# Performance work log

Measured on AMD Instinct MI355X. Metric: run time of the kernel, lower is better.

Reference implementation:

```python
import jax, jax.numpy as jnp
import numpy as np

G, K1, K2, N, NP, EPS = 16, 128, 32, 128, 512, 1e-5

def _bn(x, axes):
    m = jnp.mean(x, axes, keepdims=True)
    v = jnp.var(x, axes, keepdims=True)  # biased, as torch BN training mode
    return (x - m) * jax.lax.rsqrt(v + EPS)

def _fps(xyz, npoint):
    # farthest point sampling, deterministic start at index 0; xyz (B,P,3)
    B, P, _ = xyz.shape
    def step(carry, _):
        dists, far = carry
        c = jnp.take_along_axis(xyz, far[:, None, None], axis=1)   # (B,1,3)
        d = jnp.sum((xyz - c) ** 2, -1)                            # (B,P)
        dists = jnp.minimum(dists, d)
        return (dists, jnp.argmax(dists, -1)), far
    init = (jnp.full((B, P), 1e10, xyz.dtype), jnp.zeros((B,), jnp.int32))
    _, idx = jax.lax.scan(step, init, None, length=npoint)         # (npoint,B)
    return jnp.take_along_axis(xyz, idx.T[:, :, None], axis=1)     # (B,npoint,3)

def _pointnet(x, w1, b1, w2, b2, w3, b3):
    h = jax.nn.relu(_bn(x @ w1 + b1, (0, 1)))
    h = jax.nn.relu(_bn(h @ w2 + b2, (0, 1)))
    h = _bn(h @ w3 + b3, (0, 1))
    return jnp.max(h, axis=1)                                      # (B,1024)

def _mapping(feat, w1, b1, w2, b2, w3, b3, w4, b4):
    # all 16 branches stacked on leading axis g
    h = jax.nn.relu(_bn(jnp.einsum('bk,gkj->gbj', feat, w1) + b1[:, None, :], (1,)))
    h = jax.nn.relu(_bn(jnp.einsum('gbj,gjk->gbk', h, w2) + b2[:, None, :], (1,)))
    h = jax.nn.relu(_bn(jnp.einsum('gbj,gjk->gbk', h, w3) + b3[:, None, :], (1,)))
    return jax.nn.relu(_bn(jnp.einsum('gbj,gjk->gbk', h, w4) + b4[:, None, :], (1,)))

def _axform(feat, fw, fb, c1w, c1b, c2w, c2b, c3w, c3b, c4w, c4b):
    # feat (G,B,K1); 1x1 convs expressed as einsums in channels-last layout
    xb = (jnp.einsum('gbk,gkm->gbm', feat, fw) + fb[:, None, :]).reshape(G, -1, N, K2)
    h = jax.nn.relu(_bn(jnp.einsum('gbnk,gkc->gbnc', xb, c1w) + c1b[:, None, None, :], (1, 2)))
    h = jax.nn.relu(_bn(jnp.einsum('gbnc,gcd->gbnd', h, c2w) + c2b[:, None, None, :], (1, 2)))
    h = jnp.einsum('gbnd,gde->gbne', h, c3w) + c3b[:, None, None, :]  # (G,B,N,1024)
    w = jax.nn.softmax(h, axis=2)                                     # softmax over N
    y = jnp.einsum('gbne,gbnk->gbek', w, xb)                          # (G,B,1024,K2)
    return jnp.einsum('gbek,gkc->gbec', y, c4w) + c4b[:, None, None, :]  # (G,B,1024,3)

def _forward(x, pn, mp, gen, ref):
    x_partial = _fps(x, NP)                                           # (B,512,3)
    feat = _pointnet(x, *pn)                                          # (B,1024)
    mfeat = _mapping(feat, *mp)                                       # (G,B,K1)
    x1g = _axform(mfeat, *gen)                                        # (G,B,1024,3)
    B = x.shape[0]
    x_1 = jnp.transpose(x1g, (1, 0, 2, 3)).reshape(B, -1, 3)          # (B,16384,3)
    fps1 = jax.vmap(lambda p: _fps(p, NP))(x1g)                       # (G,B,512,3)
    x_base = jnp.concatenate([fps1, jnp.broadcast_to(x_partial, (G,) + x_partial.shape)], axis=2)
    x2g = x_base + _axform(mfeat, *ref)                               # (G,B,1024,3)
    x_2 = jnp.transpose(x2g, (1, 0, 2, 3)).reshape(B, -1, 3)
    return x_1, x_2

def setup_inputs() -> dict:
    keys = iter(jax.random.split(jax.random.key(0), 40))
    def rn(shape, s=0.02):
        return (s * jax.random.normal(next(keys), shape)).astype(jnp.float32)
    inp = {}
    inp['x'] = jax.random.normal(next(keys), (16, 2048, 3), jnp.float32)
    inp['pn_w1'] = rn((3, 64));      inp['pn_b1'] = rn((64,))
    inp['pn_w2'] = rn((64, 128));    inp['pn_b2'] = rn((128,))
    inp['pn_w3'] = rn((128, 1024));  inp['pn_b3'] = rn((1024,))
    inp['mp_w1'] = rn((G, 1024, 1024)); inp['mp_b1'] = rn((G, 1024))
    inp['mp_w2'] = rn((G, 1024, 1024)); inp['mp_b2'] = rn((G, 1024))
    inp['mp_w3'] = rn((G, 1024, 1024)); inp['mp_b3'] = rn((G, 1024))
    inp['mp_w4'] = rn((G, 1024, K1));   inp['mp_b4'] = rn((G, K1))
    for p in ('g', 'r'):
        inp[p + '_fw'] = rn((G, K1, N * K2)); inp[p + '_fb'] = rn((G, N * K2))
        inp[p + '_c1w'] = rn((G, K2, 64));    inp[p + '_c1b'] = rn((G, 64))
        inp[p + '_c2w'] = rn((G, 64, 128));   inp[p + '_c2b'] = rn((G, 128))
        inp[p + '_c3w'] = rn((G, 128, 1024)); inp[p + '_c3b'] = rn((G, 1024))
        inp[p + '_c4w'] = rn((G, K2, 3));     inp[p + '_c4b'] = rn((G, 3))
    return inp

def reference(x, pn_w1, pn_b1, pn_w2, pn_b2, pn_w3, pn_b3,
              mp_w1, mp_b1, mp_w2, mp_b2, mp_w3, mp_b3, mp_w4, mp_b4,
              g_fw, g_fb, g_c1w, g_c1b, g_c2w, g_c2b, g_c3w, g_c3b, g_c4w, g_c4b,
              r_fw, r_fb, r_c1w, r_c1b, r_c2w, r_c2b, r_c3w, r_c3b, r_c4w, r_c4b):
    pn = (pn_w1, pn_b1, pn_w2, pn_b2, pn_w3, pn_b3)
    mp = (mp_w1, mp_b1, mp_w2, mp_b2, mp_w3, mp_b3, mp_w4, mp_b4)
    gen = (g_fw, g_fb, g_c1w, g_c1b, g_c2w, g_c2b, g_c3w, g_c3b, g_c4w, g_c4b)
    ref = (r_fw, r_fb, r_c1w, r_c1b, r_c2w, r_c2b, r_c3w, r_c3b, r_c4w, r_c4b)
    return _forward(x, pn, mp, gen, ref)
```

## Files before the change

kernel.cpp:

```cpp
#include <hip/hip_runtime.h>
#include <math.h>

#define TID ((int)threadIdx.x)

namespace {
constexpr float EPSf = 1e-5f;

struct FpsArgs {
  const float* pts; float* out; float* dmin; int* far;
  int it0, it1, nc;
};

__device__ __forceinline__ unsigned fenc(float f){
  unsigned u = __float_as_uint(f);
  return (u & 0x80000000u) ? ~u : (u | 0x80000000u);
}
__device__ __forceinline__ float fdec(unsigned e){
  unsigned u = (e & 0x80000000u) ? (e & 0x7fffffffu) : ~e;
  return __uint_as_float(u);
}

template<int CTRL>
__device__ __forceinline__ void dpp_comb(float& bm, int& bp){
  int om_i = __builtin_amdgcn_update_dpp(__float_as_int(bm), __float_as_int(bm), CTRL, 0xf, 0xf, false);
  int op   = __builtin_amdgcn_update_dpp(bp, bp, CTRL, 0xf, 0xf, false);
  float om = __int_as_float(om_i);
  if (om > bm || (om == bm && op < bp)){ bm = om; bp = op; }
}

template<int LP>
__device__ void fps_body(const FpsArgs& a, int ci){
  const int NPTS = 256*LP;
  const float* pts = a.pts + (size_t)ci * NPTS * 3;
  float* out = a.out + (size_t)ci * 512 * 3;
  float* dst = a.dmin + (size_t)ci * NPTS;
  float px[LP], py[LP], pz[LP], dmin[LP];
#pragma unroll
  for (int j = 0; j < LP; j++){
    int p = TID + 256*j;
    px[j] = pts[p*3+0]; py[j] = pts[p*3+1]; pz[j] = pts[p*3+2];
  }
  int far;
  if (a.it0 == 0){
#pragma unroll
    for (int j = 0; j < LP; j++) dmin[j] = 1e10f;
    far = 0;
  } else {
#pragma unroll
    for (int j = 0; j < LP; j++) dmin[j] = dst[TID + 256*j];
    far = a.far[ci];
  }
  __shared__ unsigned long long red2[2][4];
  for (int i = a.it0; i < a.it1; i++){
    float cx = pts[far*3+0], cy = pts[far*3+1], cz = pts[far*3+2];
    if (TID == 0){ out[i*3+0]=cx; out[i*3+1]=cy; out[i*3+2]=cz; }
    float bm = -1.f; int bp = 0;
#pragma unroll
    for (int j = 0; j < LP; j++){
      float dx = __fsub_rn(px[j], cx);
      float dy = __fsub_rn(py[j], cy);
      float dz = __fsub_rn(pz[j], cz);
      float d  = __fadd_rn(__fadd_rn(__fmul_rn(dx,dx), __fmul_rn(dy,dy)), __fmul_rn(dz,dz));
      float dm = fminf(dmin[j], d);
      dmin[j] = dm;
      if (dm > bm){ bm = dm; bp = TID + 256*j; }
    }
    dpp_comb<0x111>(bm,bp); dpp_comb<0x112>(bm,bp); dpp_comb<0x114>(bm,bp);
    dpp_comb<0x118>(bm,bp); dpp_comb<0x142>(bm,bp); dpp_comb<0x143>(bm,bp);
    unsigned long long key =
      ((unsigned long long)(unsigned)__builtin_amdgcn_readlane(__float_as_int(bm), 63) << 32)
      | (unsigned)~(unsigned)__builtin_amdgcn_readlane(bp, 63);
    if ((TID & 63) == 63) red2[i&1][TID>>6] = key;
    __syncthreads();
    unsigned long long k0=red2[i&1][0], k1=red2[i&1][1], k2=red2[i&1][2], k3=red2[i&1][3];
    k0 = k0>k1?k0:k1; k2 = k2>k3?k2:k3; k0 = k0>k2?k0:k2;
    far = (int)~(unsigned)k0;
  }
  if (a.it1 < 512){
#pragma unroll
    for (int j = 0; j < LP; j++) dst[TID + 256*j] = dmin[j];
    if (TID == 0) a.far[ci] = far;
  }
}

__device__ __forceinline__ int aswz64(int n, int k){
  return (n << 6) + ((((k >> 2) ^ ((n >> 3) & 3)) << 2) | (k & 3));
}
__device__ __forceinline__ int pswz(int n, int e){
  return (n << 6) + (e ^ (((n >> 3) & 3) << 3));
}

template<int C, int K, int FLP>
__global__ void __launch_bounds__(256) rowgemm_kernel(const float* __restrict__ in,
    const float* __restrict__ w, const float* __restrict__ bias, const float2* __restrict__ st2,
    float* __restrict__ out, int rows_per_g, FpsArgs fa)
{
  int bid = blockIdx.x;
  if constexpr (FLP > 0){
    if (bid < fa.nc){ fps_body<FLP>(fa, bid); return; }
    bid -= fa.nc;
  }
  constexpr int RPB = 256 / C;
  __shared__ float lin[RPB * K];
  size_t row0 = (size_t)bid * RPB;
  int g = (int)(row0 / rows_per_g);
  for (int i = TID; i < RPB*K; i += 256){
    float v = in[row0*(size_t)K + i];
    if (st2){ float2 s = st2[(size_t)g*K + (i % K)]; v = fmaxf((v - s.x)*s.y, 0.f); }
    lin[i] = v;
  }
  __syncthreads();
  int r = TID / C, c = TID % C;
  float acc = bias[(size_t)g*C + c];
  const float* wg = w + (size_t)g*K*C + c;
#pragma unroll
  for (int k = 0; k < K; k++) acc = fmaf(lin[r*K + k], wg[(size_t)k*C], acc);
  out[(row0 + r)*C + c] = acc;
}

template<int FLP>
__global__ void __launch_bounds__(256) big1024_kernel(const float* __restrict__ in,
    const float* __restrict__ w, const float* __restrict__ bias, const float2* __restrict__ st2,
    float* __restrict__ ps, float* __restrict__ pq,
    unsigned* __restrict__ maxenc, int rows_per_g, FpsArgs fa)
{
  int bid = blockIdx.x;
  if constexpr (FLP > 0){
    if (bid < fa.nc){ fps_body<FLP>(fa, bid); return; }
    bid -= fa.nc;
  }
  int rb = bid >> 1, ch = bid & 1;
  __shared__ float lin[32 * 128];
  size_t row0 = (size_t)rb * 32;
  int g = (int)(row0 / rows_per_g);
  for (int i = TID; i < 32*128; i += 256){
    float v = in[row0*128 + i];
    if (st2){ float2 s = st2[(size_t)g*128 + (i & 127)]; v = fmaxf((v - s.x)*s.y, 0.f); }
    lin[i] = v;
  }
  __syncthreads();
  int c0 = ch*512 + TID, c1 = c0 + 256;
  float a0[32], a1[32];
  float b0 = bias[(size_t)g*1024 + c0], b1 = bias[(size_t)g*1024 + c1];
#pragma unroll
  for (int r = 0; r < 32; r++){ a0[r] = b0; a1[r] = b1; }
  const float* wg = w + (size_t)g*128*1024;
  for (int k = 0; k < 128; k++){
    float w0 = wg[(size_t)k*1024 + c0];
    float w1 = wg[(size_t)k*1024 + c1];
#pragma unroll
    for (int r = 0; r < 32; r++){
      float lv = lin[r*128 + k];
      a0[r] = fmaf(lv, w0, a0[r]);
      a1[r] = fmaf(lv, w1, a1[r]);
    }
  }
  int b = (int)(row0 / 2048);
  float s0=0.f,q0=0.f,m0=-1e38f,s1=0.f,q1=0.f,m1=-1e38f;
#pragma unroll
  for (int r = 0; r < 32; r++){
    s0 += a0[r]; q0 = fmaf(a0[r],a0[r],q0); m0 = fmaxf(m0, a0[r]);
    s1 += a1[r]; q1 = fmaf(a1[r],a1[r],q1); m1 = fmaxf(m1, a1[r]);
  }
  ps[(size_t)rb*1024 + c0] = s0; pq[(size_t)rb*1024 + c0] = q0;
  ps[(size_t)rb*1024 + c1] = s1; pq[(size_t)rb*1024 + c1] = q1;
  atomicMax(&maxenc[(size_t)b*1024 + c0], fenc(m0));
  atomicMax(&maxenc[(size_t)b*1024 + c1], fenc(m1));
}

template<int FLP>
__global__ void __launch_bounds__(256) mapgemm_kernel(const float* __restrict__ in, int in_gstride,
    const float* __restrict__ w, const float* __restrict__ bias, const float2* __restrict__ st2,
    float* __restrict__ out, int K, int J, int JB, int NS, FpsArgs fa)
{
  int bid = blockIdx.x;
  if constexpr (FLP > 0){
    if (bid < fa.nc){ fps_body<FLP>(fa, bid); return; }
    bid -= fa.nc;
  }
  int kc = bid / (JB*16);
  int g  = (bid / JB) % 16;
  int jb = bid % JB;
  int j  = jb*256 + TID;
  bool jv = j < J;
  int jc = jv ? j : 0;
  int kchunk = K / NS;
  int k0 = kc * kchunk;
  __shared__ float lin[16 * 128];
  const float* ing = in + (size_t)g * in_gstride;
  float acc[16];
  float bv = (NS == 1 && jv) ? bias[(size_t)g*J + jc] : 0.f;
#pragma unroll
  for (int b = 0; b < 16; b++) acc[b] = bv;
  for (int kt = k0; kt < k0 + kchunk; kt += 128){
    __syncthreads();
    for (int i = TID; i < 2048; i += 256){
      int b = i >> 7, k = i & 127;
      float v = ing[(size_t)b*K + kt + k];
      if (st2){ float2 s = st2[(size_t)g*K + kt + k]; v = fmaxf((v - s.x)*s.y, 0.f); }
      lin[i] = v;
    }
    __syncthreads();
    const float* wg = w + ((size_t)g*K + kt)*J + jc;
    for (int k = 0; k < 128; k++){
      float wv = wg[(size_t)k*J];
#pragma unroll
      for (int b = 0; b < 16; b++) acc[b] = fmaf(lin[b*128 + k], wv, acc[b]);
    }
  }
  if (jv){
    if (NS == 1){
      for (int b = 0; b < 16; b++) out[((size_t)g*16 + b)*J + j] = acc[b];
    } else {
      for (int b = 0; b < 16; b++) out[(((size_t)kc*16 + g)*16 + b)*J + j] = acc[b];
    }
  }
}

__global__ void __launch_bounds__(256) redstats_kernel(const float* __restrict__ part,
    const float* __restrict__ bias, float* __restrict__ out, float2* __restrict__ st2,
    int J, int NS)
{
  int t = blockIdx.x*256 + TID;
  int g = t / J, j = t % J;
  float bv = bias[t];
  float s = 0.f, q = 0.f;
  for (int b = 0; b < 16; b++){
    float v = bv;
    for (int c = 0; c < NS; c++) v += part[(((size_t)c*16 + g)*16 + b)*J + j];
    out[((size_t)g*16 + b)*J + j] = v;
    s += v; q = fmaf(v, v, q);
  }
  float mean = s * (1.f/16.f);
  float var  = q * (1.f/16.f) - mean*mean;
  st2[t] = make_float2(mean, rsqrtf(fmaxf(var, 0.f) + EPSf));
}

__global__ void __launch_bounds__(256) statsacc_kernel(const float* __restrict__ in,
    float* __restrict__ part, int C, size_t chunk)
{
  size_t base = (size_t)blockIdx.x * chunk;
  int c = TID % C;
  float s = 0.f, q = 0.f;
  for (size_t idx = base + TID; idx < base + chunk; idx += 256){
    float v = in[idx]; s += v; q = fmaf(v, v, q);
  }
  __shared__ float ls[256], lq[256];
  ls[TID] = s; lq[TID] = q; __syncthreads();
  if (TID < C){
    for (int t = TID + C; t < 256; t += C){ s += ls[t]; q += lq[t]; }
    part[((size_t)blockIdx.x*C + c)*2]   = s;
    part[((size_t)blockIdx.x*C + c)*2+1] = q;
  }
}

__global__ void statsfin_kernel(const float* __restrict__ part, float2* __restrict__ st2,
    int C, int G, float invR)
{
  int slot = blockIdx.x*256 + TID;
  if (slot >= G*C) return;
  int g = slot / C, c = slot % C;
  int bpg = 256 / G;
  float s = 0.f, q = 0.f;
  for (int b = 0; b < bpg; b++){
    size_t p = ((size_t)(g*bpg + b)*C + c)*2;
    s += part[p]; q += part[p+1];
  }
  float mean = s*invR;
  float var  = q*invR - mean*mean;
  st2[slot] = make_float2(mean, rsqrtf(fmaxf(var, 0.f) + EPSf));
}

__global__ void pnfin_kernel(const float* __restrict__ ps, const float* __restrict__ pq,
                             float2* __restrict__ st)
{
  int c = blockIdx.x*256 + TID;
  float s = 0.f, q = 0.f;
  for (int rb = 0; rb < 1024; rb++){ s += ps[rb*1024 + c]; q += pq[rb*1024 + c]; }
  float mean = s * (1.f/32768.f);
  float var  = q * (1.f/32768.f) - mean*mean;
  st[c] = make_float2(mean, rsqrtf(fmaxf(var, 0.f) + EPSf));
}

__global__ void feat_kernel(const unsigned* __restrict__ me, const float2* __restrict__ st,
                            float* __restrict__ feat)
{
  int t = blockIdx.x*256 + TID;
  int c = t & 1023;
  float2 s = st[c];
  feat[t] = (fdec(me[t]) - s.x) * s.y;
}

template<int FLP>
__global__ void __launch_bounds__(256, 4) fused_kernel(const float* __restrict__ c2o,
    const float2* __restrict__ st2, const float* __restrict__ c3w,
    const float* __restrict__ xb, const float* __restrict__ c4w, const float* __restrict__ c4b,
    float* __restrict__ out_pts, float* __restrict__ out_x1, FpsArgs fa)
{
  int bid = blockIdx.x;
  if constexpr (FLP > 0){
    if (bid < fa.nc){ fps_body<FLP>(fa, bid); return; }
    bid -= fa.nc;
  }
  int gb = bid >> 3, eb = bid & 7;
  int g = gb >> 4, b = gb & 15;
  __shared__ float As[8192];
  __shared__ float xbl[4096];
  for (int i = TID; i < 4096; i += 256) xbl[i] = xb[(size_t)gb*4096 + i];

  int tn = TID >> 4, te = TID & 15;
  int n0 = tn*8, e0 = te*8;
  const float* wgp = c3w + ((size_t)g << 17) + eb*128 + e0;
  const float* src = c2o + (size_t)gb*16384;
  float h[8][8];
#pragma unroll
  for (int i = 0; i < 8; i++)
#pragma unroll
    for (int j = 0; j < 8; j++) h[i][j] = 0.f;

  for (int kh = 0; kh < 2; kh++){
    __syncthreads();
    for (int i = TID; i < 8192; i += 256){
      int n = i >> 6, k = i & 63;
      int kg = kh*64 + k;
      float2 s = st2[(size_t)g*128 + kg];
      As[aswz64(n,k)] = fmaxf((src[n*128 + kg] - s.x)*s.y, 0.f);
    }
    __syncthreads();
    for (int k4 = 0; k4 < 64; k4 += 4){
      float4 a[8];
#pragma unroll
      for (int i = 0; i < 8; i++) a[i] = *(const float4*)&As[aswz64(n0+i, k4)];
#pragma unroll
      for (int kk = 0; kk < 4; kk++){
        float4 wa = *(const float4*)(wgp + (size_t)(kh*64 + k4 + kk)*1024);
        float4 wb = *(const float4*)(wgp + (size_t)(kh*64 + k4 + kk)*1024 + 4);
#pragma unroll
        for (int i = 0; i < 8; i++){
          float av = (&a[i].x)[kk];
          h[i][0] = fmaf(av, wa.x, h[i][0]);
          h[i][1] = fmaf(av, wa.y, h[i][1]);
          h[i][2] = fmaf(av, wa.z, h[i][2]);
          h[i][3] = fmaf(av, wa.w, h[i][3]);
          h[i][4] = fmaf(av, wb.x, h[i][4]);
          h[i][5] = fmaf(av, wb.y, h[i][5]);
          h[i][6] = fmaf(av, wb.z, h[i][6]);
          h[i][7] = fmaf(av, wb.w, h[i][7]);
        }
      }
    }
  }

  for (int p = 0; p < 2; p++){
    __syncthreads();
    if ((te >> 3) == p){
      int el0 = (te & 7) * 8;
#pragma unroll
      for (int i = 0; i < 8; i++){
#pragma unroll
        for (int j4 = 0; j4 < 8; j4 += 4)
          *(float4*)&As[pswz(n0+i, el0+j4)] =
            make_float4(h[i][j4], h[i][j4+1], h[i][j4+2], h[i][j4+3]);
      }
    }
    __syncthreads();
    if (TID < 128){
      int el = TID >> 1, hh = TID & 1;
      float m = -1e38f;
      for (int jj = 0; jj < 64; jj++){
        int n = hh*64 + jj;
        m = fmaxf(m, As[pswz(n, el)]);
      }
      m = fmaxf(m, __shfl_xor(m, 1));
      float s = 0.f;
      float4 y[8];
#pragma unroll
      for (int q = 0; q < 8; q++) y[q] = make_float4(0.f,0.f,0.f,0.f);
      for (int jj = 0; jj < 64; jj++){
        int n = hh*64 + jj;
        float wv = __expf(As[pswz(n, el)] - m);
        s += wv;
        const float4* xr = (const float4*)&xbl[n*32];
#pragma unroll
        for (int q = 0; q < 8; q++){
          float4 xv = xr[q];
          y[q].x = fmaf(wv, xv.x, y[q].x);
          y[q].y = fmaf(wv, xv.y, y[q].y);
          y[q].z = fmaf(wv, xv.z, y[q].z);
          y[q].w = fmaf(wv, xv.w, y[q].w);
        }
      }
      s += __shfl_xor(s, 1);
#pragma unroll
      for (int q = 0; q < 8; q++){
        y[q].x += __shfl_xor(y[q].x, 1);
        y[q].y += __shfl_xor(y[q].y, 1);
        y[q].z += __shfl_xor(y[q].z, 1);
        y[q].w += __shfl_xor(y[q].w, 1);
      }
      if (hh == 0){
        const float* cw = c4w + g*96;
        float o0 = 0.f, o1 = 0.f, o2 = 0.f;
#pragma unroll
        for (int q = 0; q < 8; q++){
#pragma unroll
          for (int c2 = 0; c2 < 4; c2++){
            float yv = (&y[q].x)[c2];
            int k = q*4 + c2;
            o0 = fmaf(yv, cw[k*3+0], o0);
            o1 = fmaf(yv, cw[k*3+1], o1);
            o2 = fmaf(yv, cw[k*3+2], o2);
          }
        }
        float rs = 1.f / s;
        o0 = fmaf(rs, o0, c4b[g*3+0]);
        o1 = fmaf(rs, o1, c4b[g*3+1]);
        o2 = fmaf(rs, o2, c4b[g*3+2]);
        int eg = eb*128 + p*64 + el;
        size_t po = ((size_t)gb*1024 + eg)*3;
        out_pts[po+0] = o0; out_pts[po+1] = o1; out_pts[po+2] = o2;
        if (out_x1){
          size_t xo = (((size_t)b*16 + g)*1024 + eg)*3;
          out_x1[xo+0] = o0; out_x1[xo+1] = o1; out_x1[xo+2] = o2;
        }
      }
    }
  }
}

__global__ void combine_kernel(const float* __restrict__ fps1, const float* __restrict__ xpart,
                               const float* __restrict__ d2, float* __restrict__ x2)
{
  size_t i = (size_t)blockIdx.x*256 + TID;
  if (i >= (size_t)16*16*1024*3) return;
  int c = (int)(i % 3);
  size_t t = i / 3;
  int e = (int)(t % 1024);
  size_t gb = t / 1024;
  int g = (int)(gb >> 4), b = (int)(gb & 15);
  float base;
  if (e < 512) base = fps1[(gb*512 + e)*3 + c];
  else         base = xpart[((size_t)b*512 + (e - 512))*3 + c];
  x2[(((size_t)b*16384) + (size_t)g*1024 + e)*3 + c] = base + d2[i];
}

}

extern "C" void kernel_launch(void* const* d_in, const int* in_sizes, int n_in,
                              void* d_out, int out_size, void* d_ws, size_t ws_size,
                              hipStream_t stream)
{
  (void)in_sizes; (void)n_in; (void)out_size; (void)ws_size;
  const float* x    = (const float*)d_in[0];
  const float* pnw1 = (const float*)d_in[1];
  const float* pnb1 = (const float*)d_in[2];
  const float* pnw2 = (const float*)d_in[3];
  const float* pnb2 = (const float*)d_in[4];
  const float* pnw3 = (const float*)d_in[5];
  const float* pnb3 = (const float*)d_in[6];
  const float* mpw[4] = {(const float*)d_in[7],(const float*)d_in[9],(const float*)d_in[11],(const float*)d_in[13]};
  const float* mpb[4] = {(const float*)d_in[8],(const float*)d_in[10],(const float*)d_in[12],(const float*)d_in[14]};

  float* ws = (float*)d_ws;
  size_t o = 0;
  auto alloc = [&](size_t n){ float* p = ws + o; o += n; return p; };
  float* x_partial = alloc(24576);
  float* feat      = alloc(16384);
  float* mfeat     = alloc(32768);
  float2* st_pn1   = (float2*)alloc(128);
  float2* st_pn2   = (float2*)alloc(256);
  float2* st_pn3   = (float2*)alloc(2048);
  float2* st_c1    = (float2*)alloc(2048);
  float2* st_c2    = (float2*)alloc(4096);
  float2* st_map0  = (float2*)alloc(32768);
  float2* st_map1  = (float2*)alloc(32768);
  float2* st_map2  = (float2*)alloc(32768);
  float2* st_map3  = (float2*)alloc(4096);
  float* sa_part   = alloc(65536);
  float* pn_ps     = alloc(1048576);
  float* pn_pq     = alloc(1048576);
  unsigned* maxenc = (unsigned*)alloc(16384);
  float* mapA      = alloc(262144);
  float* mapB      = alloc(262144);
  float* mpart     = alloc(1048576);
  float* xb        = alloc(1048576);
  float* c1o       = alloc(2097152);
  float* c2o       = alloc(4194304);
  float* x1g       = alloc(786432);
  float* d2buf     = alloc(786432);
  float* fps1b     = alloc(393216);
  float* fpsA_dmin = alloc(32768);
  int*   fpsA_far  = (int*)alloc(16);
  float* fpsB_dmin = alloc(262144);
  int*   fpsB_far  = (int*)alloc(256);

  float* xout1 = (float*)d_out;
  float* xout2 = xout1 + 786432;

  hipMemsetAsync(maxenc, 0, 16384*sizeof(unsigned), stream);

  FpsArgs f0{};
  FpsArgs fa{x, x_partial, fpsA_dmin, fpsA_far, 0, 96, 16};

  rowgemm_kernel<64,3,8><<<8192+16, 256, 0, stream>>>(x, pnw1, pnb1, nullptr, c1o, 32768, fa);
  statsacc_kernel<<<256, 256, 0, stream>>>(c1o, sa_part, 64, 8192);
  statsfin_kernel<<<1, 256, 0, stream>>>(sa_part, st_pn1, 64, 1, 1.f/32768.f);
  fa.it0 = 96; fa.it1 = 256;
  rowgemm_kernel<128,64,8><<<16384+16, 256, 0, stream>>>(c1o, pnw2, pnb2, st_pn1, c2o, 32768, fa);
  statsacc_kernel<<<256, 256, 0, stream>>>(c2o, sa_part, 128, 16384);
  statsfin_kernel<<<1, 256, 0, stream>>>(sa_part, st_pn2, 128, 1, 1.f/32768.f);
  fa.it0 = 256; fa.it1 = 512;
  big1024_kernel<8><<<2048+16, 256, 0, stream>>>(c2o, pnw3, pnb3, st_pn2,
                                                 pn_ps, pn_pq, maxenc, 32768, fa);
  pnfin_kernel<<<4, 256, 0, stream>>>(pn_ps, pn_pq, st_pn3);
  feat_kernel<<<64, 256, 0, stream>>>(maxenc, st_pn3, feat);

  mapgemm_kernel<0><<<256, 256, 0, stream>>>(feat, 0,     mpw[0], nullptr, nullptr, mpart, 1024, 1024, 4, 4, f0);
  redstats_kernel<<<64, 256, 0, stream>>>(mpart, mpb[0], mapA, st_map0, 1024, 4);
  mapgemm_kernel<0><<<256, 256, 0, stream>>>(mapA, 16384, mpw[1], nullptr, st_map0, mpart, 1024, 1024, 4, 4, f0);
  redstats_kernel<<<64, 256, 0, stream>>>(mpart, mpb[1], mapB, st_map1, 1024, 4);
  mapgemm_kernel<0><<<256, 256, 0, stream>>>(mapB, 16384, mpw[2], nullptr, st_map1, mpart, 1024, 1024, 4, 4, f0);
  redstats_kernel<<<64, 256, 0, stream>>>(mpart, mpb[2], mapA, st_map2, 1024, 4);
  mapgemm_kernel<0><<<64, 256, 0, stream>>>(mapA, 16384, mpw[3], nullptr, st_map2, mpart, 1024, 128, 1, 4, f0);
  redstats_kernel<<<8, 256, 0, stream>>>(mpart, mpb[3], mfeat, st_map3, 128, 4);

  for (int p = 0; p < 2; p++){
    const float* fw  = (const float*)d_in[15 + p*10 + 0];
    const float* fb  = (const float*)d_in[15 + p*10 + 1];
    const float* c1w = (const float*)d_in[15 + p*10 + 2];
    const float* c1b = (const float*)d_in[15 + p*10 + 3];
    const float* c2w = (const float*)d_in[15 + p*10 + 4];
    const float* c2b = (const float*)d_in[15 + p*10 + 5];
    const float* c3w = (const float*)d_in[15 + p*10 + 6];
    const float* c4w = (const float*)d_in[15 + p*10 + 8];
    const float* c4b = (const float*)d_in[15 + p*10 + 9];

    if (p == 0){
      mapgemm_kernel<0><<<256, 256, 0, stream>>>(mfeat, 2048, fw, fb, st_map3, xb, 128, 4096, 16, 1, f0);
      rowgemm_kernel<64,32,0><<<8192, 256, 0, stream>>>(xb, c1w, c1b, nullptr, c1o, 2048, f0);
      statsacc_kernel<<<256, 256, 0, stream>>>(c1o, sa_part, 64, 8192);
      statsfin_kernel<<<4, 256, 0, stream>>>(sa_part, st_c1, 64, 16, 1.f/2048.f);
      rowgemm_kernel<128,64,0><<<16384, 256, 0, stream>>>(c1o, c2w, c2b, st_c1, c2o, 2048, f0);
      statsacc_kernel<<<256, 256, 0, stream>>>(c2o, sa_part, 128, 16384);
      statsfin_kernel<<<8, 256, 0, stream>>>(sa_part, st_c2, 128, 16, 1.f/2048.f);
      fused_kernel<0><<<2048, 256, 0, stream>>>(c2o, st_c2, c3w, xb, c4w, c4b, x1g, xout1, f0);
    } else {
      FpsArgs fb_{x1g, fps1b, fpsB_dmin, fpsB_far, 0, 64, 256};
      mapgemm_kernel<4><<<256+256, 256, 0, stream>>>(mfeat, 2048, fw, fb, st_map3, xb, 128, 4096, 16, 1, fb_);
      fb_.it0 = 64; fb_.it1 = 128;
      rowgemm_kernel<64,32,4><<<8192+256, 256, 0, stream>>>(xb, c1w, c1b, nullptr, c1o, 2048, fb_);
      statsacc_kernel<<<256, 256, 0, stream>>>(c1o, sa_part, 64, 8192);
      statsfin_kernel<<<4, 256, 0, stream>>>(sa_part, st_c1, 64, 16, 1.f/2048.f);
      fb_.it0 = 128; fb_.it1 = 256;
      rowgemm_kernel<128,64,4><<<16384+256, 256, 0, stream>>>(c1o, c2w, c2b, st_c1, c2o, 2048, fb_);
      statsacc_kernel<<<256, 256, 0, stream>>>(c2o, sa_part, 128, 16384);
      statsfin_kernel<<<8, 256, 0, stream>>>(sa_part, st_c2, 128, 16, 1.f/2048.f);
      fb_.it0 = 256; fb_.it1 = 512;
      fused_kernel<4><<<2048+256, 256, 0, stream>>>(c2o, st_c2, c3w, xb, c4w, c4b, d2buf, nullptr, fb_);
    }
  }

  combine_kernel<<<3072, 256, 0, stream>>>(fps1b, x_partial, d2buf, xout2);
}
```

Before: 1.899 ms.

## Register-tile pointnet 1024 GEMM, split-K mapping GEMMs, and respread FPS across kernels

The 1024-wide pointnet GEMM now uses an 8x8 register tile per thread over transposed shared inputs with float4 weight loads, and reduces per-column stats through shared memory before the atomics. The mapping GEMMs move to a new 128-thread kernel with 16-way split-K and float4 outputs, which needs a larger partial buffer. The FPS iterations for the first point cloud are spread over more launches, including the mapping and first-branch kernels, and the second FPS schedule is rebalanced. The aim is better data reuse, more parallelism in the small GEMMs, and hiding the serial FPS latency behind more of the work. The cost is more shared-memory syncs and a larger split-K reduction in redstats.

```diff
diff --git a/kernel.cpp b/kernel.cpp
--- a/kernel.cpp
+++ b/kernel.cpp
@@ -28,16 +28,16 @@
   if (om > bm || (om == bm && op < bp)){ bm = om; bp = op; }
 }
 
-template<int LP>
+template<int LP, int NT>
 __device__ void fps_body(const FpsArgs& a, int ci){
-  const int NPTS = 256*LP;
+  const int NPTS = NT*LP;
   const float* pts = a.pts + (size_t)ci * NPTS * 3;
   float* out = a.out + (size_t)ci * 512 * 3;
   float* dst = a.dmin + (size_t)ci * NPTS;
   float px[LP], py[LP], pz[LP], dmin[LP];
 #pragma unroll
   for (int j = 0; j < LP; j++){
-    int p = TID + 256*j;
+    int p = TID + NT*j;
     px[j] = pts[p*3+0]; py[j] = pts[p*3+1]; pz[j] = pts[p*3+2];
   }
   int far;
@@ -47,10 +47,10 @@
     far = 0;
   } else {
 #pragma unroll
-    for (int j = 0; j < LP; j++) dmin[j] = dst[TID + 256*j];
+    for (int j = 0; j < LP; j++) dmin[j] = dst[TID + NT*j];
     far = a.far[ci];
   }
-  __shared__ unsigned long long red2[2][4];
+  __shared__ unsigned long long red2[2][NT/64];
   for (int i = a.it0; i < a.it1; i++){
     float cx = pts[far*3+0], cy = pts[far*3+1], cz = pts[far*3+2];
     if (TID == 0){ out[i*3+0]=cx; out[i*3+1]=cy; out[i*3+2]=cz; }
@@ -63,7 +63,7 @@
       float d  = __fadd_rn(__fadd_rn(__fmul_rn(dx,dx), __fmul_rn(dy,dy)), __fmul_rn(dz,dz));
       float dm = fminf(dmin[j], d);
       dmin[j] = dm;
-      if (dm > bm){ bm = dm; bp = TID + 256*j; }
+      if (dm > bm){ bm = dm; bp = TID + NT*j; }
     }
     dpp_comb<0x111>(bm,bp); dpp_comb<0x112>(bm,bp); dpp_comb<0x114>(bm,bp);
     dpp_comb<0x118>(bm,bp); dpp_comb<0x142>(bm,bp); dpp_comb<0x143>(bm,bp);
@@ -72,13 +72,17 @@
       | (unsigned)~(unsigned)__builtin_amdgcn_readlane(bp, 63);
     if ((TID & 63) == 63) red2[i&1][TID>>6] = key;
     __syncthreads();
-    unsigned long long k0=red2[i&1][0], k1=red2[i&1][1], k2=red2[i&1][2], k3=red2[i&1][3];
-    k0 = k0>k1?k0:k1; k2 = k2>k3?k2:k3; k0 = k0>k2?k0:k2;
-    far = (int)~(unsigned)k0;
+    unsigned long long kk = red2[i&1][0];
+#pragma unroll
+    for (int t = 1; t < NT/64; t++){
+      unsigned long long o = red2[i&1][t];
+      kk = kk > o ? kk : o;
+    }
+    far = (int)~(unsigned)kk;
   }
   if (a.it1 < 512){
 #pragma unroll
-    for (int j = 0; j < LP; j++) dst[TID + 256*j] = dmin[j];
+    for (int j = 0; j < LP; j++) dst[TID + NT*j] = dmin[j];
     if (TID == 0) a.far[ci] = far;
   }
 }
@@ -97,7 +101,7 @@
 {
   int bid = blockIdx.x;
   if constexpr (FLP > 0){
-    if (bid < fa.nc){ fps_body<FLP>(fa, bid); return; }
+    if (bid < fa.nc){ fps_body<FLP,256>(fa, bid); return; }
     bid -= fa.nc;
   }
   constexpr int RPB = 256 / C;
@@ -119,65 +123,162 @@
 }
 
 template<int FLP>
-__global__ void __launch_bounds__(256) big1024_kernel(const float* __restrict__ in,
+__global__ void __launch_bounds__(256, 4) big1024b_kernel(const float* __restrict__ in,
     const float* __restrict__ w, const float* __restrict__ bias, const float2* __restrict__ st2,
-    float* __restrict__ ps, float* __restrict__ pq,
-    unsigned* __restrict__ maxenc, int rows_per_g, FpsArgs fa)
+    float* __restrict__ ps, float* __restrict__ pq, unsigned* __restrict__ maxenc, FpsArgs fa)
 {
   int bid = blockIdx.x;
   if constexpr (FLP > 0){
-    if (bid < fa.nc){ fps_body<FLP>(fa, bid); return; }
+    if (bid < fa.nc){ fps_body<FLP,256>(fa, bid); return; }
     bid -= fa.nc;
   }
   int rb = bid >> 1, ch = bid & 1;
-  __shared__ float lin[32 * 128];
   size_t row0 = (size_t)rb * 32;
-  int g = (int)(row0 / rows_per_g);
-  for (int i = TID; i < 32*128; i += 256){
-    float v = in[row0*128 + i];
-    if (st2){ float2 s = st2[(size_t)g*128 + (i & 127)]; v = fmaxf((v - s.x)*s.y, 0.f); }
-    lin[i] = v;
+  __shared__ float linT[4096];
+  for (int i = TID; i < 4096; i += 256){
+    int r = i >> 7, k = i & 127;
+    float v = in[(row0 + r)*128 + k];
+    float2 s = st2[k];
+    linT[k*32 + r] = fmaxf((v - s.x)*s.y, 0.f);
   }
   __syncthreads();
-  int c0 = ch*512 + TID, c1 = c0 + 256;
-  float a0[32], a1[32];
-  float b0 = bias[(size_t)g*1024 + c0], b1 = bias[(size_t)g*1024 + c1];
-#pragma unroll
-  for (int r = 0; r < 32; r++){ a0[r] = b0; a1[r] = b1; }
-  const float* wg = w + (size_t)g*128*1024;
+  int rq = TID >> 6, cq = TID & 63;
+  int c0 = ch*512 + cq*8;
+  float acc[8][8];
+  {
+    float4 b0 = *(const float4*)(bias + c0);
+    float4 b1 = *(const float4*)(bias + c0 + 4);
+    const float bv[8] = {b0.x,b0.y,b0.z,b0.w,b1.x,b1.y,b1.z,b1.w};
+#pragma unroll
+    for (int ri = 0; ri < 8; ri++)
+#pragma unroll
+      for (int ci = 0; ci < 8; ci++) acc[ri][ci] = bv[ci];
+  }
+  const float* wp = w + c0;
+#pragma unroll 2
   for (int k = 0; k < 128; k++){
-    float w0 = wg[(size_t)k*1024 + c0];
-    float w1 = wg[(size_t)k*1024 + c1];
-#pragma unroll
-    for (int r = 0; r < 32; r++){
-      float lv = lin[r*128 + k];
-      a0[r] = fmaf(lv, w0, a0[r]);
-      a1[r] = fmaf(lv, w1, a1[r]);
-    }
-  }
-  int b = (int)(row0 / 2048);
-  float s0=0.f,q0=0.f,m0=-1e38f,s1=0.f,q1=0.f,m1=-1e38f;
-#pragma unroll
-  for (int r = 0; r < 32; r++){
-    s0 += a0[r]; q0 = fmaf(a0[r],a0[r],q0); m0 = fmaxf(m0, a0[r]);
-    s1 += a1[r]; q1 = fmaf(a1[r],a1[r],q1); m1 = fmaxf(m1, a1[r]);
-  }
-  ps[(size_t)rb*1024 + c0] = s0; pq[(size_t)rb*1024 + c0] = q0;
-  ps[(size_t)rb*1024 + c1] = s1; pq[(size_t)rb*1024 + c1] = q1;
-  atomicMax(&maxenc[(size_t)b*1024 + c0], fenc(m0));
-  atomicMax(&maxenc[(size_t)b*1024 + c1], fenc(m1));
+    float4 w0 = *(const float4*)(wp + (size_t)k*1024);
+    float4 w1 = *(const float4*)(wp + (size_t)k*1024 + 4);
+    float4 l0 = *(const float4*)&linT[k*32 + rq*8];
+    float4 l1 = *(const float4*)&linT[k*32 + rq*8 + 4];
+    const float lv[8] = {l0.x,l0.y,l0.z,l0.w,l1.x,l1.y,l1.z,l1.w};
+    const float wv[8] = {w0.x,w0.y,w0.z,w0.w,w1.x,w1.y,w1.z,w1.w};
+#pragma unroll
+    for (int ri = 0; ri < 8; ri++)
+#pragma unroll
+      for (int ci = 0; ci < 8; ci++)
+        acc[ri][ci] = fmaf(lv[ri], wv[ci], acc[ri][ci]);
+  }
+  float s[8], q[8], m[8];
+#pragma unroll
+  for (int ci = 0; ci < 8; ci++){
+    s[ci] = 0.f; q[ci] = 0.f; m[ci] = -1e38f;
+#pragma unroll
+    for (int ri = 0; ri < 8; ri++){
+      float v = acc[ri][ci];
+      s[ci] += v; q[ci] = fmaf(v, v, q[ci]); m[ci] = fmaxf(m[ci], v);
+    }
+  }
+  __syncthreads();
+  float* red = linT;
+#pragma unroll
+  for (int ci = 0; ci < 8; ci++){
+    red[rq*512 + cq*8 + ci]        = s[ci];
+    red[2048 + rq*512 + cq*8 + ci] = q[ci];
+  }
+  __syncthreads();
+  if (rq == 0){
+#pragma unroll
+    for (int ci = 0; ci < 8; ci++){
+      float ss = 0.f, qq = 0.f;
+#pragma unroll
+      for (int r = 0; r < 4; r++){
+        ss += red[r*512 + cq*8 + ci];
+        qq += red[2048 + r*512 + cq*8 + ci];
+      }
+      ps[(size_t)rb*1024 + c0 + ci] = ss;
+      pq[(size_t)rb*1024 + c0 + ci] = qq;
+    }
+  }
+  __syncthreads();
+#pragma unroll
+  for (int ci = 0; ci < 8; ci++) red[rq*512 + cq*8 + ci] = m[ci];
+  __syncthreads();
+  if (rq == 0){
+    int b = (int)(row0 / 2048);
+#pragma unroll
+    for (int ci = 0; ci < 8; ci++){
+      float mm = red[cq*8 + ci];
+#pragma unroll
+      for (int r = 1; r < 4; r++) mm = fmaxf(mm, red[r*512 + cq*8 + ci]);
+      atomicMax(&maxenc[(size_t)b*1024 + c0 + ci], fenc(mm));
+    }
+  }
 }
 
 template<int FLP>
+__global__ void __launch_bounds__(128) mapgemm2_kernel(const float* __restrict__ in, int in_gstride,
+    const float* __restrict__ w, const float* __restrict__ bias, const float2* __restrict__ st2,
+    float* __restrict__ out, int K, int J, int JB, int NS, FpsArgs fa)
+{
+  int bid = blockIdx.x;
+  if constexpr (FLP > 0){
+    if (bid < fa.nc){ fps_body<FLP,128>(fa, bid); return; }
+    bid -= fa.nc;
+  }
+  int kc = bid / (JB*16);
+  int g  = (bid / JB) % 16;
+  int jb = bid % JB;
+  int kchunk = K / NS, k0 = kc*kchunk;
+  __shared__ float linT[128*16];
+  const float* ing = in + (size_t)g * in_gstride;
+  for (int i = TID; i < kchunk*16; i += 128){
+    int b = i / kchunk, k = i - b*kchunk;
+    float v = ing[(size_t)b*K + k0 + k];
+    if (st2){ float2 s = st2[(size_t)g*K + k0 + k]; v = fmaxf((v - s.x)*s.y, 0.f); }
+    linT[k*16 + b] = v;
+  }
+  __syncthreads();
+  int bh = TID >> 6, jq = TID & 63;
+  int j = jb*256 + jq*4;
+  const float* wp = w + ((size_t)g*K + k0)*J + j;
+  float4 a4[8];
+#pragma unroll
+  for (int bi = 0; bi < 8; bi++) a4[bi] = make_float4(0.f,0.f,0.f,0.f);
+#pragma unroll 4
+  for (int k = 0; k < kchunk; k++){
+    float4 wv = *(const float4*)(wp + (size_t)k*J);
+    float4 l0 = *(const float4*)&linT[k*16 + bh*8];
+    float4 l1 = *(const float4*)&linT[k*16 + bh*8 + 4];
+    const float lv[8] = {l0.x,l0.y,l0.z,l0.w,l1.x,l1.y,l1.z,l1.w};
+#pragma unroll
+    for (int bi = 0; bi < 8; bi++){
+      a4[bi].x = fmaf(lv[bi], wv.x, a4[bi].x);
+      a4[bi].y = fmaf(lv[bi], wv.y, a4[bi].y);
+      a4[bi].z = fmaf(lv[bi], wv.z, a4[bi].z);
+      a4[bi].w = fmaf(lv[bi], wv.w, a4[bi].w);
+    }
+  }
+  if (NS == 1){
+    float4 bv = *(const float4*)(bias + (size_t)g*J + j);
+#pragma unroll
+    for (int bi = 0; bi < 8; bi++){
+      int b = bh*8 + bi;
+      float4 o = make_float4(a4[bi].x+bv.x, a4[bi].y+bv.y, a4[bi].z+bv.z, a4[bi].w+bv.w);
+      *(float4*)&out[((size_t)g*16 + b)*J + j] = o;
+    }
+  } else {
+#pragma unroll
+    for (int bi = 0; bi < 8; bi++)
+      *(float4*)&out[(((size_t)kc*16 + g)*16 + bh*8 + bi)*J + j] = a4[bi];
+  }
+}
+
 __global__ void __launch_bounds__(256) mapgemm_kernel(const float* __restrict__ in, int in_gstride,
     const float* __restrict__ w, const float* __restrict__ bias, const float2* __restrict__ st2,
-    float* __restrict__ out, int K, int J, int JB, int NS, FpsArgs fa)
+    float* __restrict__ out, int K, int J, int JB, int NS)
 {
   int bid = blockIdx.x;
-  if constexpr (FLP > 0){
-    if (bid < fa.nc){ fps_body<FLP>(fa, bid); return; }
-    bid -= fa.nc;
-  }
   int kc = bid / (JB*16);
   int g  = (bid / JB) % 16;
   int jb = bid % JB;
@@ -299,7 +400,7 @@
 {
   int bid = blockIdx.x;
   if constexpr (FLP > 0){
-    if (bid < fa.nc){ fps_body<FLP>(fa, bid); return; }
+    if (bid < fa.nc){ fps_body<FLP,256>(fa, bid); return; }
     bid -= fa.nc;
   }
   int gb = bid >> 3, eb = bid & 7;
@@ -482,7 +583,7 @@
   unsigned* maxenc = (unsigned*)alloc(16384);
   float* mapA      = alloc(262144);
   float* mapB      = alloc(262144);
-  float* mpart     = alloc(1048576);
+  float* mpart     = alloc(4194304);
   float* xb        = alloc(1048576);
   float* c1o       = alloc(2097152);
   float* c2o       = alloc(4194304);
@@ -500,28 +601,32 @@
   hipMemsetAsync(maxenc, 0, 16384*sizeof(unsigned), stream);
 
   FpsArgs f0{};
-  FpsArgs fa{x, x_partial, fpsA_dmin, fpsA_far, 0, 96, 16};
-
+  FpsArgs fa{x, x_partial, fpsA_dmin, fpsA_far, 0, 0, 16};
+
+  fa.it0 = 0; fa.it1 = 64;
   rowgemm_kernel<64,3,8><<<8192+16, 256, 0, stream>>>(x, pnw1, pnb1, nullptr, c1o, 32768, fa);
   statsacc_kernel<<<256, 256, 0, stream>>>(c1o, sa_part, 64, 8192);
   statsfin_kernel<<<1, 256, 0, stream>>>(sa_part, st_pn1, 64, 1, 1.f/32768.f);
-  fa.it0 = 96; fa.it1 = 256;
+  fa.it0 = 64; fa.it1 = 128;
   rowgemm_kernel<128,64,8><<<16384+16, 256, 0, stream>>>(c1o, pnw2, pnb2, st_pn1, c2o, 32768, fa);
   statsacc_kernel<<<256, 256, 0, stream>>>(c2o, sa_part, 128, 16384);
   statsfin_kernel<<<1, 256, 0, stream>>>(sa_part, st_pn2, 128, 1, 1.f/32768.f);
-  fa.it0 = 256; fa.it1 = 512;
-  big1024_kernel<8><<<2048+16, 256, 0, stream>>>(c2o, pnw3, pnb3, st_pn2,
-                                                 pn_ps, pn_pq, maxenc, 32768, fa);
+  fa.it0 = 128; fa.it1 = 224;
+  big1024b_kernel<8><<<2048+16, 256, 0, stream>>>(c2o, pnw3, pnb3, st_pn2,
+                                                  pn_ps, pn_pq, maxenc, fa);
   pnfin_kernel<<<4, 256, 0, stream>>>(pn_ps, pn_pq, st_pn3);
   feat_kernel<<<64, 256, 0, stream>>>(maxenc, st_pn3, feat);
 
-  mapgemm_kernel<0><<<256, 256, 0, stream>>>(feat, 0,     mpw[0], nullptr, nullptr, mpart, 1024, 1024, 4, 4, f0);
-  redstats_kernel<<<64, 256, 0, stream>>>(mpart, mpb[0], mapA, st_map0, 1024, 4);
-  mapgemm_kernel<0><<<256, 256, 0, stream>>>(mapA, 16384, mpw[1], nullptr, st_map0, mpart, 1024, 1024, 4, 4, f0);
-  redstats_kernel<<<64, 256, 0, stream>>>(mpart, mpb[1], mapB, st_map1, 1024, 4);
-  mapgemm_kernel<0><<<256, 256, 0, stream>>>(mapB, 16384, mpw[2], nullptr, st_map1, mpart, 1024, 1024, 4, 4, f0);
-  redstats_kernel<<<64, 256, 0, stream>>>(mpart, mpb[2], mapA, st_map2, 1024, 4);
-  mapgemm_kernel<0><<<64, 256, 0, stream>>>(mapA, 16384, mpw[3], nullptr, st_map2, mpart, 1024, 128, 1, 4, f0);
+  fa.it0 = 224; fa.it1 = 288;
+  mapgemm2_kernel<16><<<1024+16, 128, 0, stream>>>(feat, 0,     mpw[0], nullptr, nullptr, mpart, 1024, 1024, 4, 16, fa);
+  redstats_kernel<<<64, 256, 0, stream>>>(mpart, mpb[0], mapA, st_map0, 1024, 16);
+  fa.it0 = 288; fa.it1 = 352;
+  mapgemm2_kernel<16><<<1024+16, 128, 0, stream>>>(mapA, 16384, mpw[1], nullptr, st_map0, mpart, 1024, 1024, 4, 16, fa);
+  redstats_kernel<<<64, 256, 0, stream>>>(mpart, mpb[1], mapB, st_map1, 1024, 16);
+  fa.it0 = 352; fa.it1 = 416;
+  mapgemm2_kernel<16><<<1024+16, 128, 0, stream>>>(mapB, 16384, mpw[2], nullptr, st_map1, mpart, 1024, 1024, 4, 16, fa);
+  redstats_kernel<<<64, 256, 0, stream>>>(mpart, mpb[2], mapA, st_map2, 1024, 16);
+  mapgemm_kernel<<<64, 256, 0, stream>>>(mapA, 16384, mpw[3], nullptr, st_map2, mpart, 1024, 128, 1, 4);
   redstats_kernel<<<8, 256, 0, stream>>>(mpart, mpb[3], mfeat, st_map3, 128, 4);
 
   for (int p = 0; p < 2; p++){
@@ -536,8 +641,10 @@
     const float* c4b = (const float*)d_in[15 + p*10 + 9];
 
     if (p == 0){
-      mapgemm_kernel<0><<<256, 256, 0, stream>>>(mfeat, 2048, fw, fb, st_map3, xb, 128, 4096, 16, 1, f0);
-      rowgemm_kernel<64,32,0><<<8192, 256, 0, stream>>>(xb, c1w, c1b, nullptr, c1o, 2048, f0);
+      fa.it0 = 416; fa.it1 = 480;
+      mapgemm2_kernel<16><<<256+16, 128, 0, stream>>>(mfeat, 2048, fw, fb, st_map3, xb, 128, 4096, 16, 1, fa);
+      fa.it0 = 480; fa.it1 = 512;
+      rowgemm_kernel<64,32,8><<<8192+16, 256, 0, stream>>>(xb, c1w, c1b, nullptr, c1o, 2048, fa);
       statsacc_kernel<<<256, 256, 0, stream>>>(c1o, sa_part, 64, 8192);
       statsfin_kernel<<<4, 256, 0, stream>>>(sa_part, st_c1, 64, 16, 1.f/2048.f);
       rowgemm_kernel<128,64,0><<<16384, 256, 0, stream>>>(c1o, c2w, c2b, st_c1, c2o, 2048, f0);
@@ -545,17 +652,17 @@
       statsfin_kernel<<<8, 256, 0, stream>>>(sa_part, st_c2, 128, 16, 1.f/2048.f);
       fused_kernel<0><<<2048, 256, 0, stream>>>(c2o, st_c2, c3w, xb, c4w, c4b, x1g, xout1, f0);
     } else {
-      FpsArgs fb_{x1g, fps1b, fpsB_dmin, fpsB_far, 0, 64, 256};
-      mapgemm_kernel<4><<<256+256, 256, 0, stream>>>(mfeat, 2048, fw, fb, st_map3, xb, 128, 4096, 16, 1, fb_);
-      fb_.it0 = 64; fb_.it1 = 128;
+      FpsArgs fb_{x1g, fps1b, fpsB_dmin, fpsB_far, 0, 0, 256};
+      mapgemm2_kernel<0><<<256, 128, 0, stream>>>(mfeat, 2048, fw, fb, st_map3, xb, 128, 4096, 16, 1, f0);
+      fb_.it0 = 0; fb_.it1 = 64;
       rowgemm_kernel<64,32,4><<<8192+256, 256, 0, stream>>>(xb, c1w, c1b, nullptr, c1o, 2048, fb_);
       statsacc_kernel<<<256, 256, 0, stream>>>(c1o, sa_part, 64, 8192);
       statsfin_kernel<<<4, 256, 0, stream>>>(sa_part, st_c1, 64, 16, 1.f/2048.f);
-      fb_.it0 = 128; fb_.it1 = 256;
+      fb_.it0 = 64; fb_.it1 = 160;
       rowgemm_kernel<128,64,4><<<16384+256, 256, 0, stream>>>(c1o, c2w, c2b, st_c1, c2o, 2048, fb_);
       statsacc_kernel<<<256, 256, 0, stream>>>(c2o, sa_part, 128, 16384);
       statsfin_kernel<<<8, 256, 0, stream>>>(sa_part, st_c2, 128, 16, 1.f/2048.f);
-      fb_.it0 = 256; fb_.it1 = 512;
+      fb_.it0 = 160; fb_.it1 = 512;
       fused_kernel<4><<<2048+256, 256, 0, stream>>>(c2o, st_c2, c3w, xb, c4w, c4b, d2buf, nullptr, fb_);
     }
   }
```

After: 1.955 ms. 1.03x slower.
